# Kernel tuning notes

Hardware: AMD Instinct MI355X
Metric: run time of the kernel (lower is better)

## Reference

```python
import jax, jax.numpy as jnp
import numpy as np

D_MODEL, D_STATE, B, S = 1024, 64, 8, 2048


def setup_inputs() -> dict:
    key = jax.random.key(0)
    ks = jax.random.split(key, 14)
    inp = {"x": jax.random.normal(ks[0], (B, S, D_MODEL), jnp.float32)}
    names = ["cog", "beh", "env", "delta", "Bp", "Cp"]
    for i, n in enumerate(names):
        inp[f"W_{n}"] = jax.random.normal(ks[1 + 2 * i], (D_STATE, D_MODEL), jnp.float32) / np.sqrt(D_MODEL)
        inp[f"b_{n}"] = jnp.zeros((D_STATE,), jnp.float32)
    # torch init is log(|randn|+1e-4); we use strictly-negative A_log so the
    # length-2048 multiplicative recurrence stays finite (A_log is a learned
    # parameter, so its value is free; the math of forward is unchanged).
    inp["A_log"] = -jnp.abs(jax.random.normal(ks[13], (D_STATE, D_STATE), jnp.float32)) - 0.1
    return inp


def reference(x, W_cog, b_cog, W_beh, b_beh, W_env, b_env,
              W_delta, b_delta, W_Bp, b_Bp, W_Cp, b_Cp, A_log):
    # gating terms (computed in the source but never used downstream)
    A_t = (jax.nn.sigmoid(x @ W_cog.T + b_cog)
           * jax.nn.sigmoid(x @ W_beh.T + b_beh)
           * jax.nn.sigmoid(x @ W_env.T + b_env))
    del A_t

    delta = jax.nn.softplus(x @ W_delta.T + b_delta)   # [B,S,N]
    Bt = x @ W_Bp.T + b_Bp                             # [B,S,N]
    Ct = x @ W_Cp.T + b_Cp                             # [B,S,N]
    u = Bt * x[:, :, :D_STATE]                         # [B,S,N]

    # Faithful to torch broadcasting: after step 0 the carried state h is
    # [B,N,N] with h[b,i,j] = exp(A_log[i,j]*delta[b,t,i]) * h_prev[b,i,j] + u[b,t,j]
    def step(h, td):
        d, u_t, c_t = td                               # each [B,N]
        A = jnp.exp(A_log[None, :, :] * d[:, :, None]) # [B,N,N]
        h = A * h + u_t[:, None, :]
        y = jnp.einsum('bj,bij->bi', c_t, h)           # [B,N]
        return h, y

    h0 = jnp.zeros((x.shape[0], D_STATE, D_STATE), x.dtype)
    _, ys = jax.lax.scan(
        step, h0,
        (delta.transpose(1, 0, 2), u.transpose(1, 0, 2), Ct.transpose(1, 0, 2)))
    # torch stacks y_t of shape [B,1,N] along dim=1 -> [B,S,1,N]
    return ys.transpose(1, 0, 2)[:, :, None, :]
```

## Files before the change

kernel.cpp:

```cpp
#include <hip/hip_runtime.h>
#include <math.h>

#define DM   1024
#define DS   64
#define BATCH 8
#define SEQ  2048
#define CL   32
#define NC   64

typedef __bf16 bf16x8 __attribute__((ext_vector_type(8)));
typedef float  f32x4  __attribute__((ext_vector_type(4)));

#if __has_builtin(__builtin_amdgcn_exp2f)
#define EXP2(v) __builtin_amdgcn_exp2f(v)
#else
#define EXP2(v) __expf(0.69314718056f * (v))
#endif

__global__ __launch_bounds__(256) void wconv_kernel(
    const float* __restrict__ Wd, const float* __restrict__ Wb,
    const float* __restrict__ Wc, __bf16* __restrict__ Wp)
{
    int idx = blockIdx.x * 256 + threadIdx.x;
    int k  = idx & 1023;
    int n  = idx >> 10;
    const float* W = (n < 64) ? Wd : (n < 128 ? Wb : Wc);
    float v = W[(size_t)(n & 63) * DM + k];
    int kt = k >> 5, kk = k & 31;
    Wp[((size_t)kt * 192 + n) * 32 + kk] = (__bf16)v;
}

__global__ __launch_bounds__(256, 2) void projp1_full(
    const float* __restrict__ x, const __bf16* __restrict__ Wp,
    const float* __restrict__ bd, const float* __restrict__ bb,
    const float* __restrict__ bc, const float* __restrict__ A_log,
    float* __restrict__ delta_g, float* __restrict__ u_g,
    float* __restrict__ ct_g,
    float* __restrict__ E, float* __restrict__ Dsum)
{
    __shared__ __bf16 sB[2][12288];
    __shared__ __bf16 sA[2][32 * 72];
    __shared__ float  s_d[CL * 64];
    __shared__ float  s_u[CL * 64];

    const int tid  = threadIdx.x;
    const int row0 = blockIdx.x * 32;

    const int lane = tid & 63, wv = tid >> 6;
    const int l15  = lane & 15, quad = lane >> 4;
    const int nbase = wv * 48;

    const int am = tid >> 3;
    const int ak = tid & 7;
    const float* xga = x + (size_t)(row0 + am) * DM + ak * 8;

    f32x4 acc[2][3];
    #pragma unroll
    for (int mt = 0; mt < 2; ++mt)
        #pragma unroll
        for (int nt = 0; nt < 3; ++nt)
            acc[mt][nt] = (f32x4){0.f, 0.f, 0.f, 0.f};

    float4 areg[2];

#if __has_builtin(__builtin_amdgcn_global_load_lds)
    #define LOADB(kb, bi) do {                                                \
        _Pragma("unroll")                                                     \
        for (int it = 0; it < 6; ++it) {                                      \
            const __bf16* gsrc =                                              \
                Wp + (size_t)(kb) * 12288 + (tid + it * 256) * 8;             \
            __bf16* ldst = &sB[bi][(tid + it * 256) * 8];                     \
            __builtin_amdgcn_global_load_lds(                                 \
                (const __attribute__((address_space(1))) void*)gsrc,          \
                (__attribute__((address_space(3))) void*)ldst, 16, 0, 0);     \
        }                                                                     \
    } while (0)
#else
    #define LOADB(kb, bi) do {                                                \
        _Pragma("unroll")                                                     \
        for (int it = 0; it < 6; ++it) {                                      \
            uint4 t = *(const uint4*)(                                        \
                Wp + (size_t)(kb) * 12288 + (tid + it * 256) * 8);            \
            *(uint4*)&sB[bi][(tid + it * 256) * 8] = t;                       \
        }                                                                     \
    } while (0)
#endif
    #define LOADA(kb) do {                                                    \
        areg[0] = *(const float4*)(xga + (kb) * 64);                          \
        areg[1] = *(const float4*)(xga + (kb) * 64 + 4);                      \
    } while (0)
    #define STAGEA(bi) do {                                                   \
        bf16x8 hv = {(__bf16)areg[0].x, (__bf16)areg[0].y,                    \
                     (__bf16)areg[0].z, (__bf16)areg[0].w,                    \
                     (__bf16)areg[1].x, (__bf16)areg[1].y,                    \
                     (__bf16)areg[1].z, (__bf16)areg[1].w};                   \
        *(bf16x8*)&sA[bi][am * 72 + ak * 8] = hv;                             \
    } while (0)
    #define COMPUTE(bi) do {                                                  \
        _Pragma("unroll")                                                     \
        for (int s = 0; s < 2; ++s) {                                         \
            bf16x8 af[2];                                                     \
            _Pragma("unroll")                                                 \
            for (int mt = 0; mt < 2; ++mt)                                    \
                af[mt] = *(const bf16x8*)                                     \
                    &sA[bi][(mt * 16 + l15) * 72 + s * 32 + quad * 8];        \
            _Pragma("unroll")                                                 \
            for (int nt = 0; nt < 3; ++nt) {                                  \
                bf16x8 bv = *(const bf16x8*)                                  \
                    &sB[bi][s * 6144 + (nbase + nt * 16 + l15) * 32           \
                            + quad * 8];                                      \
                _Pragma("unroll")                                             \
                for (int mt = 0; mt < 2; ++mt)                                \
                    acc[mt][nt] = __builtin_amdgcn_mfma_f32_16x16x32_bf16(    \
                        af[mt], bv, acc[mt][nt], 0, 0, 0);                    \
            }                                                                 \
        }                                                                     \
    } while (0)

    LOADB(0, 0);
    LOADA(0);
    STAGEA(0);
    __syncthreads();

    int buf = 0;
    for (int kb = 0; kb < 16; ++kb) {
        if (kb < 15) {
            LOADB(kb + 1, buf ^ 1);
            LOADA(kb + 1);
        }
        COMPUTE(buf);
        if (kb < 15) STAGEA(buf ^ 1);
        __syncthreads();
        buf ^= 1;
    }
    #undef LOADB
    #undef LOADA
    #undef STAGEA
    #undef COMPUTE

    #pragma unroll
    for (int nt = 0; nt < 3; ++nt) {
        int gn  = nbase + nt * 16 + l15;
        int mat = (nbase + nt * 16) >> 6;
        int col = gn & 63;
        float bias = (mat == 0) ? bd[col] : (mat == 1 ? bb[col] : bc[col]);
        #pragma unroll
        for (int mt = 0; mt < 2; ++mt) {
            #pragma unroll
            for (int r = 0; r < 4; ++r) {
                int tl = mt * 16 + quad * 4 + r;
                int m  = row0 + tl;
                float v = acc[mt][nt][r] + bias;
                if (mat == 0) {
                    float sp = (v > 20.f) ? v : __logf(1.f + __expf(v));
                    delta_g[(size_t)m * DS + col] = sp;
                    s_d[tl * 64 + col] = sp;
                } else if (mat == 1) {
                    float uu = v * x[(size_t)m * DM + col];
                    u_g[(size_t)m * DS + col] = uu;
                    s_u[tl * 64 + col] = uu;
                } else {
                    ct_g[(size_t)m * DS + col] = v;
                }
            }
        }
    }
    __syncthreads();

    const int bidx = row0 >> 11;
    const int cidx = (row0 >> 5) & 63;
    const int si = tid & 63;
    const int sj = tid >> 6;

    float alog[16];
    {
        const float4* ar = (const float4*)(A_log + si * 64 + sj * 16);
        #pragma unroll
        for (int qq = 0; qq < 4; ++qq) {
            float4 v = ar[qq];
            alog[4*qq+0] = v.x * 1.44269504f; alog[4*qq+1] = v.y * 1.44269504f;
            alog[4*qq+2] = v.z * 1.44269504f; alog[4*qq+3] = v.w * 1.44269504f;
        }
    }

    float h[16];
    #pragma unroll
    for (int k = 0; k < 16; ++k) h[k] = 0.f;
    float dsum = 0.f;

    for (int t = 0; t < CL; ++t) {
        float d = s_d[t * 64 + si];
        dsum += d;
        const float* up = s_u + t * 64 + sj * 16;
        #pragma unroll
        for (int k = 0; k < 16; ++k)
            h[k] = EXP2(alog[k] * d) * h[k] + up[k];
    }

    float* eo = E + (((size_t)cidx * BATCH + bidx) * 64 + si) * 64 + sj * 16;
    #pragma unroll
    for (int qq = 0; qq < 4; ++qq)
        ((float4*)eo)[qq] = make_float4(h[4*qq], h[4*qq+1], h[4*qq+2], h[4*qq+3]);
    if (sj == 0) Dsum[((size_t)cidx * BATCH + bidx) * 64 + si] = dsum;
}

__device__ __forceinline__ void scan_range(
    const float* __restrict__ Eb, const float* __restrict__ Db,
    int n0, int n1, int bb_, int i_, int jg_,
    const float* __restrict__ alog, float* __restrict__ h)
{
    if (n0 >= n1) return;
    size_t idx = ((size_t)n0 * BATCH + bb_) * 64 + i_;
    float dsA = Db[idx];
    const float4* ep = (const float4*)(Eb + idx * 64 + jg_ * 16);
    float4 e0 = ep[0], e1 = ep[1], e2 = ep[2], e3 = ep[3];
    for (int n = n0; n < n1; ++n) {
        float dsN = 0.f;
        float4 f0 = make_float4(0.f,0.f,0.f,0.f), f1 = f0, f2 = f0, f3 = f0;
        if (n + 1 < n1) {
            size_t idx2 = ((size_t)(n + 1) * BATCH + bb_) * 64 + i_;
            dsN = Db[idx2];
            const float4* fp = (const float4*)(Eb + idx2 * 64 + jg_ * 16);
            f0 = fp[0]; f1 = fp[1]; f2 = fp[2]; f3 = fp[3];
        }
        float ev[16] = {e0.x,e0.y,e0.z,e0.w, e1.x,e1.y,e1.z,e1.w,
                        e2.x,e2.y,e2.z,e2.w, e3.x,e3.y,e3.z,e3.w};
        #pragma unroll
        for (int k = 0; k < 16; ++k)
            h[k] = EXP2(alog[k] * dsA) * h[k] + ev[k];
        dsA = dsN; e0 = f0; e1 = f1; e2 = f2; e3 = f3;
    }
}

__global__ __launch_bounds__(256) void group_kernel(
    const float* __restrict__ E, const float* __restrict__ Dsum,
    const float* __restrict__ A_log,
    float* __restrict__ Eg, float* __restrict__ Dg)
{
    const int g2 = blockIdx.x >> 3, b2 = blockIdx.x & 7;
    const int tid = threadIdx.x;
    const int i  = tid >> 2;
    const int jg = tid & 3;

    float alog[16];
    {
        const float4* ar = (const float4*)(A_log + i * 64 + jg * 16);
        #pragma unroll
        for (int qq = 0; qq < 4; ++qq) {
            float4 v = ar[qq];
            alog[4*qq+0] = v.x * 1.44269504f; alog[4*qq+1] = v.y * 1.44269504f;
            alog[4*qq+2] = v.z * 1.44269504f; alog[4*qq+3] = v.w * 1.44269504f;
        }
    }

    float hg[16];
    #pragma unroll
    for (int k = 0; k < 16; ++k) hg[k] = 0.f;
    scan_range(E, Dsum, g2 * 8, g2 * 8 + 8, b2, i, jg, alog, hg);

    float4* ego = (float4*)(Eg + (((size_t)g2 * BATCH + b2) * 64 + i) * 64 + jg * 16);
    ego[0] = make_float4(hg[0],  hg[1],  hg[2],  hg[3]);
    ego[1] = make_float4(hg[4],  hg[5],  hg[6],  hg[7]);
    ego[2] = make_float4(hg[8],  hg[9],  hg[10], hg[11]);
    ego[3] = make_float4(hg[12], hg[13], hg[14], hg[15]);
    if (jg == 0) {
        float Dacc = 0.f;
        #pragma unroll
        for (int q = 0; q < 8; ++q)
            Dacc += Dsum[((size_t)(g2 * 8 + q) * BATCH + b2) * 64 + i];
        Dg[((size_t)g2 * BATCH + b2) * 64 + i] = Dacc;
    }
}

__global__ __launch_bounds__(256) void pass23_kernel(
    const float* __restrict__ delta_g, const float* __restrict__ u_g,
    const float* __restrict__ ct_g, const float* __restrict__ A_log,
    const float* __restrict__ E, const float* __restrict__ Dsum,
    const float* __restrict__ Eg, const float* __restrict__ Dg,
    float* __restrict__ out)
{
    __shared__ float s_d[CL * 64];
    __shared__ float s_u[CL * 64];
    __shared__ float s_c[CL * 64];

    const int c = blockIdx.x, b = blockIdx.y, tid = threadIdx.x;
    const int t0 = c * CL;

    const float4* dg = (const float4*)(delta_g + ((size_t)b * SEQ + t0) * DS);
    const float4* ug = (const float4*)(u_g     + ((size_t)b * SEQ + t0) * DS);
    const float4* cg = (const float4*)(ct_g    + ((size_t)b * SEQ + t0) * DS);
    #pragma unroll
    for (int it = 0; it < (CL * 64 / 4) / 256; ++it) {
        int f = tid + it * 256;
        ((float4*)s_d)[f] = dg[f];
        ((float4*)s_u)[f] = ug[f];
        ((float4*)s_c)[f] = cg[f];
    }

    const int i  = tid >> 2;
    const int jg = tid & 3;

    float alog[16];
    {
        const float4* ar = (const float4*)(A_log + i * 64 + jg * 16);
        #pragma unroll
        for (int qq = 0; qq < 4; ++qq) {
            float4 v = ar[qq];
            alog[4*qq+0] = v.x * 1.44269504f; alog[4*qq+1] = v.y * 1.44269504f;
            alog[4*qq+2] = v.z * 1.44269504f; alog[4*qq+3] = v.w * 1.44269504f;
        }
    }

    float h[16];
    #pragma unroll
    for (int k = 0; k < 16; ++k) h[k] = 0.f;
    const int g = c >> 3;
    scan_range(Eg, Dg, 0, g, b, i, jg, alog, h);
    scan_range(E, Dsum, g * 8, c, b, i, jg, alog, h);
    __syncthreads();

    for (int t = 0; t < CL; ++t) {
        float d = s_d[t * 64 + i];
        const float* up  = s_u + t * 64 + jg * 16;
        const float* cp2 = s_c + t * 64 + jg * 16;
        float part = 0.f;
        #pragma unroll
        for (int k = 0; k < 16; ++k) {
            h[k] = EXP2(alog[k] * d) * h[k] + up[k];
            part += cp2[k] * h[k];
        }
        part += __shfl_xor(part, 1);
        part += __shfl_xor(part, 2);
        if (jg == 0)
            out[((size_t)b * SEQ + t0 + t) * DS + i] = part;
    }
}

extern "C" void kernel_launch(void* const* d_in, const int* in_sizes, int n_in,
                              void* d_out, int out_size, void* d_ws, size_t ws_size,
                              hipStream_t stream)
{
    (void)in_sizes; (void)n_in; (void)out_size; (void)ws_size;
    const float* x     = (const float*)d_in[0];
    const float* Wd    = (const float*)d_in[7];
    const float* bd    = (const float*)d_in[8];
    const float* Wb    = (const float*)d_in[9];
    const float* bb    = (const float*)d_in[10];
    const float* Wc    = (const float*)d_in[11];
    const float* bc    = (const float*)d_in[12];
    const float* A_log = (const float*)d_in[13];
    float* out = (float*)d_out;

    float* ws = (float*)d_ws;
    float* delta_g = ws;
    float* u_g     = ws + 1 * 1048576;
    float* ct_g    = ws + 2 * 1048576;
    float* E       = ws + 3 * 1048576;
    float* Dsum    = ws + 5242880;
    float* Eg      = ws + 5275648;
    float* Dg      = ws + 5537792;
    __bf16* Wp     = (__bf16*)(ws + 5541888);

    wconv_kernel<<<768, 256, 0, stream>>>(Wd, Wb, Wc, Wp);
    projp1_full<<<512, 256, 0, stream>>>(
        x, Wp, bd, bb, bc, A_log, delta_g, u_g, ct_g, E, Dsum);
    group_kernel<<<64, 256, 0, stream>>>(E, Dsum, A_log, Eg, Dg);
    pass23_kernel<<<dim3(NC, BATCH), 256, 0, stream>>>(
        delta_g, u_g, ct_g, A_log, E, Dsum, Eg, Dg, out);
}
```

Before: 174.7 us.

## Load GEMM fragments directly from global into registers, drop LDS staging

The projection GEMM no longer stages x and the packed weights through shared memory with double buffering and barriers. Each wave now loads its own MFMA A and B fragments straight from global memory into registers, using a two-deep register prefetch pipeline, and the k-loop is fully unrolled. This removes LDS traffic and __syncthreads, but the four waves each reload the same x rows redundantly and register pressure rises, which may hurt occupancy.

```diff
diff --git a/kernel.cpp b/kernel.cpp
--- a/kernel.cpp
+++ b/kernel.cpp
@@ -38,8 +38,6 @@
     float* __restrict__ ct_g,
     float* __restrict__ E, float* __restrict__ Dsum)
 {
-    __shared__ __bf16 sB[2][12288];
-    __shared__ __bf16 sA[2][32 * 72];
     __shared__ float  s_d[CL * 64];
     __shared__ float  s_u[CL * 64];
 
@@ -50,9 +48,7 @@
     const int l15  = lane & 15, quad = lane >> 4;
     const int nbase = wv * 48;
 
-    const int am = tid >> 3;
-    const int ak = tid & 7;
-    const float* xga = x + (size_t)(row0 + am) * DM + ak * 8;
+    const float* xrow = x + (size_t)(row0 + l15) * DM + quad * 8;
 
     f32x4 acc[2][3];
     #pragma unroll
@@ -61,81 +57,67 @@
         for (int nt = 0; nt < 3; ++nt)
             acc[mt][nt] = (f32x4){0.f, 0.f, 0.f, 0.f};
 
-    float4 areg[2];
-
-#if __has_builtin(__builtin_amdgcn_global_load_lds)
-    #define LOADB(kb, bi) do {                                                \
+    float4 xf[2][8];
+    bf16x8 af[2][4];
+    bf16x8 bfr[2][6];
+
+    #define LOADX(dst, kb) do {                                               \
         _Pragma("unroll")                                                     \
-        for (int it = 0; it < 6; ++it) {                                      \
-            const __bf16* gsrc =                                              \
-                Wp + (size_t)(kb) * 12288 + (tid + it * 256) * 8;             \
-            __bf16* ldst = &sB[bi][(tid + it * 256) * 8];                     \
-            __builtin_amdgcn_global_load_lds(                                 \
-                (const __attribute__((address_space(1))) void*)gsrc,          \
-                (__attribute__((address_space(3))) void*)ldst, 16, 0, 0);     \
+        for (int mt = 0; mt < 2; ++mt)                                        \
+            _Pragma("unroll")                                                 \
+            for (int s = 0; s < 2; ++s) {                                     \
+                (dst)[mt*4 + s*2 + 0] = *(const float4*)(                     \
+                    xrow + (size_t)mt * 16 * DM + (kb) * 64 + s * 32);        \
+                (dst)[mt*4 + s*2 + 1] = *(const float4*)(                     \
+                    xrow + (size_t)mt * 16 * DM + (kb) * 64 + s * 32 + 4);    \
+            }                                                                 \
+    } while (0)
+    #define CVT(dst, src) do {                                               \
+        _Pragma("unroll")                                                     \
+        for (int f = 0; f < 4; ++f) {                                         \
+            float4 lo = (src)[f*2], hi = (src)[f*2 + 1];                      \
+            (dst)[f] = (bf16x8){(__bf16)lo.x, (__bf16)lo.y,                   \
+                                (__bf16)lo.z, (__bf16)lo.w,                   \
+                                (__bf16)hi.x, (__bf16)hi.y,                   \
+                                (__bf16)hi.z, (__bf16)hi.w};                  \
         }                                                                     \
     } while (0)
-#else
-    #define LOADB(kb, bi) do {                                                \
+    #define LOADBF(dst, kb) do {                                              \
         _Pragma("unroll")                                                     \
-        for (int it = 0; it < 6; ++it) {                                      \
-            uint4 t = *(const uint4*)(                                        \
-                Wp + (size_t)(kb) * 12288 + (tid + it * 256) * 8);            \
-            *(uint4*)&sB[bi][(tid + it * 256) * 8] = t;                       \
-        }                                                                     \
+        for (int s = 0; s < 2; ++s)                                           \
+            _Pragma("unroll")                                                 \
+            for (int nt = 0; nt < 3; ++nt)                                    \
+                (dst)[s*3 + nt] = *(const bf16x8*)(                           \
+                    Wp + (size_t)(kb) * 12288 + s * 6144                      \
+                       + (nbase + nt * 16 + l15) * 32 + quad * 8);            \
     } while (0)
-#endif
-    #define LOADA(kb) do {                                                    \
-        areg[0] = *(const float4*)(xga + (kb) * 64);                          \
-        areg[1] = *(const float4*)(xga + (kb) * 64 + 4);                      \
-    } while (0)
-    #define STAGEA(bi) do {                                                   \
-        bf16x8 hv = {(__bf16)areg[0].x, (__bf16)areg[0].y,                    \
-                     (__bf16)areg[0].z, (__bf16)areg[0].w,                    \
-                     (__bf16)areg[1].x, (__bf16)areg[1].y,                    \
-                     (__bf16)areg[1].z, (__bf16)areg[1].w};                   \
-        *(bf16x8*)&sA[bi][am * 72 + ak * 8] = hv;                             \
-    } while (0)
-    #define COMPUTE(bi) do {                                                  \
+    #define COMPUTE(afr, bfrr) do {                                          \
         _Pragma("unroll")                                                     \
-        for (int s = 0; s < 2; ++s) {                                         \
-            bf16x8 af[2];                                                     \
-            _Pragma("unroll")                                                 \
-            for (int mt = 0; mt < 2; ++mt)                                    \
-                af[mt] = *(const bf16x8*)                                     \
-                    &sA[bi][(mt * 16 + l15) * 72 + s * 32 + quad * 8];        \
+        for (int s = 0; s < 2; ++s)                                           \
             _Pragma("unroll")                                                 \
             for (int nt = 0; nt < 3; ++nt) {                                  \
-                bf16x8 bv = *(const bf16x8*)                                  \
-                    &sB[bi][s * 6144 + (nbase + nt * 16 + l15) * 32           \
-                            + quad * 8];                                      \
                 _Pragma("unroll")                                             \
                 for (int mt = 0; mt < 2; ++mt)                                \
                     acc[mt][nt] = __builtin_amdgcn_mfma_f32_16x16x32_bf16(    \
-                        af[mt], bv, acc[mt][nt], 0, 0, 0);                    \
+                        (afr)[mt*2 + s], (bfrr)[s*3 + nt], acc[mt][nt],       \
+                        0, 0, 0);                                             \
             }                                                                 \
-        }                                                                     \
     } while (0)
 
-    LOADB(0, 0);
-    LOADA(0);
-    STAGEA(0);
-    __syncthreads();
-
-    int buf = 0;
+    LOADX(xf[0], 0);  LOADBF(bfr[0], 0);
+    LOADX(xf[1], 1);  LOADBF(bfr[1], 1);
+    CVT(af[0], xf[0]);
+
+    #pragma unroll
     for (int kb = 0; kb < 16; ++kb) {
-        if (kb < 15) {
-            LOADB(kb + 1, buf ^ 1);
-            LOADA(kb + 1);
-        }
-        COMPUTE(buf);
-        if (kb < 15) STAGEA(buf ^ 1);
-        __syncthreads();
-        buf ^= 1;
-    }
-    #undef LOADB
-    #undef LOADA
-    #undef STAGEA
+        if (kb + 2 < 16) LOADX(xf[kb & 1], kb + 2);
+        COMPUTE(af[kb & 1], bfr[kb & 1]);
+        if (kb + 2 < 16) LOADBF(bfr[kb & 1], kb + 2);
+        if (kb + 1 < 16) CVT(af[(kb & 1) ^ 1], xf[(kb & 1) ^ 1]);
+    }
+    #undef LOADX
+    #undef CVT
+    #undef LOADBF
     #undef COMPUTE
 
     #pragma unroll
```

After: 214.1 us. +22.6%, slower.
